# Performance work log

Measured on AMD Instinct MI355X. Metric: run time of the kernel, lower is better.

## Reference

```python
import jax, jax.numpy as jnp
import numpy as np

HID = 64
L = 3
RHO = 0.3
KMIN = 64
EPS = 1e-5


def conv1x1(x, w, b):
    # x: [B,C,H,W], w: [O,C], b: [O]
    return jnp.einsum('bchw,oc->bohw', x, w) + b[None, :, None, None]


def dwconv(x, w, pad, dil):
    # depthwise conv, w: [C,1,k,k], groups = C, no bias
    return jax.lax.conv_general_dilated(
        x, w, window_strides=(1, 1), padding=[(pad, pad), (pad, pad)],
        rhs_dilation=(dil, dil), feature_group_count=x.shape[1],
        dimension_numbers=('NCHW', 'OIHW', 'NCHW'))


def conv3x3(x, w, b):
    return jax.lax.conv_general_dilated(
        x, w, (1, 1), [(1, 1), (1, 1)],
        dimension_numbers=('NCHW', 'OIHW', 'NCHW')) + b[None, :, None, None]


def bn(x, g, b):
    # training-mode BatchNorm2d: batch statistics over (B,H,W) per channel
    mu = jnp.mean(x, axis=(0, 2, 3), keepdims=True)
    var = jnp.var(x, axis=(0, 2, 3), keepdims=True)
    return g[None, :, None, None] * (x - mu) * jax.lax.rsqrt(var + EPS) + b[None, :, None, None]


def setup_inputs() -> dict:
    key = jax.random.key(0)
    ks = jax.random.split(key, 40)
    B, C, H, W = 8, 1, 224, 224
    d = {}
    d['x'] = jax.random.normal(ks[0], (B, C, H, W), jnp.float32)
    # input_proj: 1x1 conv, out = 2*HID + L + 1 = 132
    d['w_in'] = jax.random.normal(ks[1], (2 * HID + L + 1, C), jnp.float32) * 0.5
    d['b_in'] = jnp.zeros((2 * HID + L + 1,), jnp.float32)
    for l in range(L):
        ksz = 2 * l + 3
        d[f'dw{l}'] = jax.random.normal(ks[2 + 4 * l], (HID, 1, ksz, ksz), jnp.float32) / ksz
        d[f'pw{l}_w'] = jax.random.normal(ks[3 + 4 * l], (HID, HID), jnp.float32) * (1.0 / np.sqrt(HID))
        d[f'pw{l}_b'] = jnp.zeros((HID,), jnp.float32)
        d[f'bn{l}_g'] = jnp.ones((HID,), jnp.float32)
        d[f'bn{l}_b'] = jnp.zeros((HID,), jnp.float32)
    d['imp_w1'] = jax.random.normal(ks[20], (HID // 4, HID), jnp.float32) * (1.0 / np.sqrt(HID))
    d['imp_b1'] = jnp.zeros((HID // 4,), jnp.float32)
    d['imp_w2'] = jax.random.normal(ks[21], (1, HID // 4, 3, 3), jnp.float32) * 0.1
    d['imp_b2'] = jnp.zeros((1,), jnp.float32)
    d['val_w'] = jax.random.normal(ks[22], (HID, HID), jnp.float32) * (1.0 / np.sqrt(HID))
    d['val_b'] = jnp.zeros((HID,), jnp.float32)
    d['out_w'] = jax.random.normal(ks[23], (HID, HID), jnp.float32) * (1.0 / np.sqrt(HID))
    d['out_b'] = jnp.zeros((HID,), jnp.float32)
    d['fin_w'] = jax.random.normal(ks[24], (HID, HID), jnp.float32) * (1.0 / np.sqrt(HID))
    d['fin_b'] = jnp.zeros((HID,), jnp.float32)
    return d


def reference(x, w_in, b_in,
              dw0, pw0_w, pw0_b, bn0_g, bn0_b,
              dw1, pw1_w, pw1_b, bn1_g, bn1_b,
              dw2, pw2_w, pw2_b, bn2_g, bn2_b,
              imp_w1, imp_b1, imp_w2, imp_b2,
              val_w, val_b, out_w, out_b, fin_w, fin_b):
    B, C, H, W = x.shape
    F_ = conv1x1(x, w_in, b_in)                       # [B, 2*HID+L+1, H, W]
    Q = F_[:, :HID]
    K = F_[:, HID:2 * HID]
    G = F_[:, 2 * HID:]                               # [B, L+1, H, W]
    # importance network: 1x1 conv -> ReLU -> 3x3 conv -> sigmoid
    imp = jax.nn.sigmoid(conv3x3(jax.nn.relu(conv1x1(K, imp_w1, imp_b1)), imp_w2, imp_b2))  # [B,1,H,W]
    # adaptive top-k sparsification: K = max(floor(rho*H*W), K_min)
    k = max(int(RHO * H * W), KMIN)
    mask_flat = imp.reshape(B, H * W)
    _, idx = jax.lax.top_k(mask_flat, k)              # [B, k]
    sparse = jnp.zeros_like(mask_flat).at[jnp.arange(B)[:, None], idx].set(1.0)
    K_cur = K * sparse.reshape(B, 1, H, W)
    # focal levels: kernel k_l = 2*l+3, dilation d_l = 2^l, pad = (k_l//2)*d_l
    levels = [(dw0, pw0_w, pw0_b, bn0_g, bn0_b, 1),
              (dw1, pw1_w, pw1_b, bn1_g, bn1_b, 2),
              (dw2, pw2_w, pw2_b, bn2_g, bn2_b, 4)]
    focal = []
    for dw, pw_w, pw_b, g, be, dil in levels:
        ksz = dw.shape[-1]
        pad = (ksz // 2) * dil
        K_cur = jax.nn.relu(bn(conv1x1(dwconv(K_cur, dw, pad, dil), pw_w, pw_b), g, be))
        focal.append(K_cur)
    Gn = jax.nn.softmax(G, axis=1)                    # softmax over L+1 gate channels
    K_agg = Gn[:, 0:1] * focal[0] + Gn[:, 1:2] * focal[1] + Gn[:, 2:3] * focal[2]
    K_global = jnp.mean(focal[-1], axis=(2, 3), keepdims=True)  # AdaptiveAvgPool2d(1), broadcast
    K_final = K_agg + Gn[:, -1:] * K_global
    V = conv1x1(K_final, val_w, val_b)
    QV = Q * V
    # output_proj Linear over channel dim (dropout is identity in eval)
    O = jnp.einsum('bchw,oc->bohw', QV, out_w) + out_b[None, :, None, None]
    # in_channels (1) != hidden_channels -> residual via final_conv on F[:, :HID] == Q
    x_proj = conv1x1(Q, fin_w, fin_b)
    return x_proj + O
```

## Files before the change

kernel.cpp:

```cpp
#include <hip/hip_runtime.h>

#define HDIM 224
#define WDIM 224
#define PPIX 50176
#define BATCH 8
#define NPIX 401408
#define KTOP 15052
#define NELEM 25690112
#define NBLK 6272
#define NBAND 14
#define NDWBLK 7168
#define NCHUNK 49

typedef __attribute__((ext_vector_type(8))) short bf8_t;
typedef __attribute__((ext_vector_type(4))) float f4_t;
typedef __attribute__((ext_vector_type(8))) unsigned short us8_t;
typedef __attribute__((ext_vector_type(4))) unsigned short us4_t;
#define MFMA_BF16 __builtin_amdgcn_mfma_f32_16x16x32_bf16

__device__ inline unsigned short f2bf(float f) {
    unsigned int u = __float_as_uint(f);
    return (unsigned short)((u + 0x7FFFu + ((u >> 16) & 1u)) >> 16);
}
__device__ inline float bf2f(unsigned short u) {
    return __uint_as_float(((unsigned int)u) << 16);
}

__device__ inline int ldsg(int r) { return ((r >> 3) ^ r) & 7; }

__device__ inline void stage_w64(const float* __restrict__ W, char* sWc, int t) {
    int o = t >> 2, cq = t & 3, c0 = cq * 16;
    const float4* src = (const float4*)(W + o * 64 + c0);
    float4 v0 = src[0], v1 = src[1], v2 = src[2], v3 = src[3];
    bf8_t p0, p1;
    p0[0] = (short)f2bf(v0.x); p0[1] = (short)f2bf(v0.y);
    p0[2] = (short)f2bf(v0.z); p0[3] = (short)f2bf(v0.w);
    p0[4] = (short)f2bf(v1.x); p0[5] = (short)f2bf(v1.y);
    p0[6] = (short)f2bf(v1.z); p0[7] = (short)f2bf(v1.w);
    p1[0] = (short)f2bf(v2.x); p1[1] = (short)f2bf(v2.y);
    p1[2] = (short)f2bf(v2.z); p1[3] = (short)f2bf(v2.w);
    p1[4] = (short)f2bf(v3.x); p1[5] = (short)f2bf(v3.y);
    p1[6] = (short)f2bf(v3.z); p1[7] = (short)f2bf(v3.w);
    int g = ldsg(o);
    *(bf8_t*)(sWc + o * 128 + (((2 * cq) ^ g) << 4)) = p0;
    *(bf8_t*)(sWc + o * 128 + (((2 * cq + 1) ^ g) << 4)) = p1;
}

__device__ inline void mfma64(const char* sWc, const char* sPc, int l, int m0, f4_t acc[4]) {
    int lr = l & 15, lg = l >> 4;
    int ra = m0 + lr, ga = ldsg(ra);
    const char* abase = sWc + ra * 128;
    bf8_t a0 = *(const bf8_t*)(abase + ((lg ^ ga) << 4));
    bf8_t a1 = *(const bf8_t*)(abase + (((lg + 4) ^ ga) << 4));
    #pragma unroll
    for (int nt = 0; nt < 4; nt++) {
        int rb = nt * 16 + lr, gb = ldsg(rb);
        const char* bbase = sPc + rb * 128;
        bf8_t b0 = *(const bf8_t*)(bbase + ((lg ^ gb) << 4));
        bf8_t b1 = *(const bf8_t*)(bbase + (((lg + 4) ^ gb) << 4));
        f4_t c = {0.f, 0.f, 0.f, 0.f};
        c = MFMA_BF16(a0, b0, c, 0, 0, 0);
        c = MFMA_BF16(a1, b1, c, 0, 0, 0);
        acc[nt] = c;
    }
}

__global__ __launch_bounds__(256) void prep_kernel(
    const float* __restrict__ w_in, const float* __restrict__ b_in,
    const float* __restrict__ imp_w1, const float* __restrict__ imp_b1,
    const float* __restrict__ fin_w, const float* __restrict__ fin_b,
    float* __restrict__ coeffs, unsigned int* __restrict__ ghist,
    unsigned int* __restrict__ pfx, int* __restrict__ rem)
{
    int t = threadIdx.x;
    if (t < 16) {
        float a = 0.f, d = 0.f;
        for (int c = 0; c < 64; c++) {
            a += imp_w1[t * 64 + c] * w_in[64 + c];
            d += imp_w1[t * 64 + c] * b_in[64 + c];
        }
        coeffs[t] = a;
        coeffs[16 + t] = d + imp_b1[t];
    }
    if (t < 64) {
        float a = 0.f, d = 0.f;
        for (int c = 0; c < 64; c++) {
            a += fin_w[t * 64 + c] * w_in[c];
            d += fin_w[t * 64 + c] * b_in[c];
        }
        coeffs[32 + t] = a;
        coeffs[96 + t] = d + fin_b[t];
    }
    for (int i = t; i < 2048; i += 256) ghist[i] = 0u;
    if (t < BATCH) { pfx[t] = 0u; rem[t] = KTOP; }
}

__global__ __launch_bounds__(256) void imp_kernel(
    const float* __restrict__ x, const float* __restrict__ coeffs,
    const float* __restrict__ imp_w2, const float* __restrict__ imp_b2,
    float* __restrict__ imp)
{
    int idx = blockIdx.x * 256 + threadIdx.x;
    int b = idx / PPIX, p = idx % PPIX;
    int h = p / WDIM, w = p % WDIM;
    float acc = imp_b2[0];
    #pragma unroll
    for (int ky = 0; ky < 3; ky++) {
        int hh = h + ky - 1;
        float okh = (hh >= 0 && hh < HDIM) ? 1.f : 0.f;
        int hc = min(max(hh, 0), HDIM - 1);
        #pragma unroll
        for (int kx = 0; kx < 3; kx++) {
            int ww = w + kx - 1;
            float ok = okh * ((ww >= 0 && ww < WDIM) ? 1.f : 0.f);
            int wc = min(max(ww, 0), WDIM - 1);
            float xv = x[b * PPIX + hc * WDIM + wc] * ok;
            #pragma unroll
            for (int c = 0; c < 16; c++) {
                float r = fmaxf(xv * coeffs[c] + coeffs[16 + c] * ok, 0.f);
                acc += r * imp_w2[c * 9 + ky * 3 + kx];
            }
        }
    }
    imp[idx] = 1.f / (1.f + expf(-acc));
}

__global__ __launch_bounds__(256) void topk_hist(
    const float* __restrict__ imp, const unsigned int* __restrict__ pfx,
    unsigned int* __restrict__ ghist, int shift)
{
    int b = blockIdx.x / NCHUNK, ch = blockIdx.x % NCHUNK;
    int t = threadIdx.x;
    __shared__ unsigned int hist[256];
    hist[t] = 0u;
    __syncthreads();
    unsigned int prefix = pfx[b];
    unsigned int himask = (shift == 24) ? 0u : (0xFFFFFFFFu << (shift + 8));
    float4 v = ((const float4*)(imp + b * PPIX + ch * 1024))[t];
    unsigned int bb[4] = {__float_as_uint(v.x), __float_as_uint(v.y),
                          __float_as_uint(v.z), __float_as_uint(v.w)};
    #pragma unroll
    for (int k = 0; k < 4; k++)
        if ((bb[k] & himask) == prefix)
            atomicAdd(&hist[(bb[k] >> shift) & 255u], 1u);
    __syncthreads();
    unsigned int c = hist[t];
    if (c) atomicAdd(&ghist[b * 256 + t], c);
}

__global__ __launch_bounds__(256) void topk_select(
    unsigned int* __restrict__ ghist, unsigned int* __restrict__ pfx,
    int* __restrict__ rem, int shift)
{
    int b = blockIdx.x;
    int t = threadIdx.x;
    __shared__ unsigned int h[256];
    h[t] = ghist[b * 256 + t];
    ghist[b * 256 + t] = 0u;
    __syncthreads();
    if (t == 0) {
        int r = rem[b];
        unsigned int bsel = 0u;
        for (int bin = 255; bin >= 0; bin--) {
            int c = (int)h[bin];
            if (c >= r) { bsel = (unsigned int)bin; break; }
            r -= c;
        }
        rem[b] = r;
        pfx[b] |= bsel << shift;
    }
}

__global__ __launch_bounds__(256) void topk_mask1(
    const float* __restrict__ imp, const unsigned int* __restrict__ pfx,
    float* __restrict__ mask, int* __restrict__ blocktie)
{
    int b = blockIdx.x / NCHUNK, ch = blockIdx.x % NCHUNK;
    int t = threadIdx.x;
    unsigned int T = pfx[b];
    float4 v = ((const float4*)(imp + b * PPIX + ch * 1024))[t];
    unsigned int bb[4] = {__float_as_uint(v.x), __float_as_uint(v.y),
                          __float_as_uint(v.z), __float_as_uint(v.w)};
    float4 mo;
    float* mp = &mo.x;
    int cnt = 0;
    #pragma unroll
    for (int k = 0; k < 4; k++) {
        mp[k] = (bb[k] > T) ? 1.f : 0.f;
        cnt += (bb[k] == T) ? 1 : 0;
    }
    ((float4*)(mask + b * PPIX + ch * 1024))[t] = mo;
    #pragma unroll
    for (int off = 32; off > 0; off >>= 1) cnt += __shfl_down(cnt, off);
    __shared__ int ws4[4];
    int lane = t & 63, wv = t >> 6;
    if (lane == 0) ws4[wv] = cnt;
    __syncthreads();
    if (t == 0) blocktie[b * NCHUNK + ch] = ws4[0] + ws4[1] + ws4[2] + ws4[3];
}

__global__ __launch_bounds__(256) void topk_mask2(
    const float* __restrict__ imp, const unsigned int* __restrict__ pfx,
    const int* __restrict__ rem_, const int* __restrict__ blocktie,
    float* __restrict__ mask)
{
    int b = blockIdx.x;
    int t = threadIdx.x, lane = t & 63, wv = t >> 6;
    unsigned int T = pfx[b];
    int rem = rem_[b];
    __shared__ int sbase[NCHUNK], scnt[NCHUNK];
    if (t == 0) {
        int s = 0;
        for (int i = 0; i < NCHUNK; i++) {
            sbase[i] = s;
            int c = blocktie[b * NCHUNK + i];
            scnt[i] = c;
            s += c;
        }
    }
    __syncthreads();
    __shared__ int wtot[4];
    for (int ch = 0; ch < NCHUNK; ch++) {
        if (scnt[ch] == 0) continue;
        int base = sbase[ch];
        if (base >= rem) break;
        for (int g = 0; g < 4; g++) {
            int i = b * PPIX + ch * 1024 + g * 256 + t;
            int flag = (__float_as_uint(imp[i]) == T) ? 1 : 0;
            unsigned long long bal = __ballot(flag);
            if (lane == 0) wtot[wv] = __popcll(bal);
            __syncthreads();
            int wbase = 0, tot = 0;
            for (int q = 0; q < 4; q++) { int c = wtot[q]; if (q < wv) wbase += c; tot += c; }
            if (flag && base + wbase + __popcll(bal & ((1ull << lane) - 1ull)) < rem)
                mask[i] = 1.f;
            base += tot;
            __syncthreads();
        }
    }
}

__global__ __launch_bounds__(256, 4) void level0_kernel(
    const float* __restrict__ x, const float* __restrict__ mask,
    const float* __restrict__ w_in, const float* __restrict__ b_in,
    const float* __restrict__ dw_w, const float* __restrict__ pw_w,
    const float* __restrict__ pw_b,
    unsigned short* __restrict__ y_out, float* __restrict__ partials)
{
    __shared__ __align__(16) short sW[4096];
    __shared__ __align__(16) short sP[4096];
    __shared__ float sred[128];
    __shared__ float sBias[64];
    char* sWc = (char*)sW; char* sPc = (char*)sP;
    int t = threadIdx.x;
    int swz = (blockIdx.x & 7) * 784 + (blockIdx.x >> 3);
    int b = swz / 784;
    int l = t & 63, og = t >> 6;
    int p0 = (swz % 784) * 64;
    int p = p0 + l;
    int h = p / WDIM, w = p % WDIM;
    stage_w64(pw_w, sWc, t);
    if (t < 64) sBias[t] = pw_b[t];

    int rowoff[3]; float okhf[3];
    int wcs[3]; float okwf[3];
    #pragma unroll
    for (int k = 0; k < 3; k++) {
        int hh = h + k - 1;
        okhf[k] = (hh >= 0 && hh < HDIM) ? 1.f : 0.f;
        rowoff[k] = min(max(hh, 0), HDIM - 1) * WDIM;
        int ww = w + k - 1;
        okwf[k] = (ww >= 0 && ww < WDIM) ? 1.f : 0.f;
        wcs[k] = min(max(ww, 0), WDIM - 1);
    }
    float mv[9], mxv[9];
    const float* mb = mask + b * PPIX;
    const float* xb = x + b * PPIX;
    #pragma unroll
    for (int ky = 0; ky < 3; ky++) {
        #pragma unroll
        for (int kx = 0; kx < 3; kx++) {
            int a = rowoff[ky] + wcs[kx];
            float mm = mb[a] * (okhf[ky] * okwf[kx]);
            mv[ky * 3 + kx] = mm;
            mxv[ky * 3 + kx] = mm * xb[a];
        }
    }
    bf8_t pk0, pk1;
    #pragma unroll
    for (int j = 0; j < 16; j++) {
        int c = og * 16 + j;
        float wk = w_in[64 + c], bk = b_in[64 + c];
        const float* dwr = dw_w + c * 9;
        float a0 = 0.f, a1 = 0.f;
        #pragma unroll
        for (int tp = 0; tp < 9; tp++) {
            float dv = dwr[tp];
            a0 += dv * mxv[tp];
            a1 += dv * mv[tp];
        }
        unsigned short bv = f2bf(wk * a0 + bk * a1);
        if (j < 8) pk0[j] = (short)bv; else pk1[j - 8] = (short)bv;
    }
    int gl = ldsg(l);
    *(bf8_t*)(sPc + l * 128 + (((2 * og) ^ gl) << 4)) = pk0;
    *(bf8_t*)(sPc + l * 128 + (((2 * og + 1) ^ gl) << 4)) = pk1;
    __syncthreads();

    int m0 = og * 16, lr = l & 15, lg = l >> 4;
    f4_t acc[4];
    mfma64(sWc, sPc, l, m0, acc);
    unsigned short* ybase = y_out + (size_t)b * 64 * PPIX + p0;
    #pragma unroll
    for (int r = 0; r < 4; r++) {
        int o = m0 + 4 * lg + r;
        float bias = sBias[o];
        float s = 0.f, s2 = 0.f;
        #pragma unroll
        for (int nt = 0; nt < 4; nt++) {
            float yv = acc[nt][r] + bias;
            ybase[(size_t)o * PPIX + nt * 16 + lr] = f2bf(yv);
            s += yv; s2 += yv * yv;
        }
        #pragma unroll
        for (int m = 1; m < 16; m <<= 1) {
            s += __shfl_xor(s, m);
            s2 += __shfl_xor(s2, m);
        }
        if (lr == 0) { sred[2 * o] = s; sred[2 * o + 1] = s2; }
    }
    __syncthreads();
    if (t < 128) partials[(size_t)blockIdx.x * 128 + t] = sred[t];
}

template<int KSZ, int DIL>
__global__ __launch_bounds__(256, 3) void dw_kernel(
    const unsigned short* __restrict__ in, const float* __restrict__ bnp,
    const float* __restrict__ dw_w, unsigned short* __restrict__ out)
{
    constexpr int PAD = (KSZ / 2) * DIL;
    constexpr int BH = 16;
    constexpr int LR = BH + 2 * PAD;
    constexpr int SW = WDIM + 2 * PAD + 4;
    constexpr int SEG = 16 + 2 * PAD;
    __shared__ float sIn[LR * SW];

    int t = threadIdx.x;
    int swz = (blockIdx.x & 7) * (NDWBLK / 8) + (blockIdx.x >> 3);
    int bc = swz / NBAND, band = swz % NBAND;
    int c = bc & 63;
    int r0 = band * BH;
    float sc = bnp[c], sh = bnp[64 + c];
    const unsigned short* plane = in + (size_t)bc * PPIX;

    constexpr int PADC = SW - WDIM;
    for (int i = t; i < LR * PADC; i += 256) {
        int r = i / PADC, cc = i % PADC;
        int col = (cc < PAD) ? cc : (cc + WDIM);
        sIn[r * SW + col] = 0.f;
    }
    for (int i = t; i < LR * 28; i += 256) {
        int sr = i / 28, q = i % 28;
        int gr = r0 - PAD + sr;
        float4 a = {0.f, 0.f, 0.f, 0.f}, bq = {0.f, 0.f, 0.f, 0.f};
        if (gr >= 0 && gr < HDIM) {
            us8_t v = *(const us8_t*)(plane + gr * WDIM + 8 * q);
            a.x = fmaxf(sc * bf2f(v[0]) + sh, 0.f);
            a.y = fmaxf(sc * bf2f(v[1]) + sh, 0.f);
            a.z = fmaxf(sc * bf2f(v[2]) + sh, 0.f);
            a.w = fmaxf(sc * bf2f(v[3]) + sh, 0.f);
            bq.x = fmaxf(sc * bf2f(v[4]) + sh, 0.f);
            bq.y = fmaxf(sc * bf2f(v[5]) + sh, 0.f);
            bq.z = fmaxf(sc * bf2f(v[6]) + sh, 0.f);
            bq.w = fmaxf(sc * bf2f(v[7]) + sh, 0.f);
        }
        *(float4*)(sIn + sr * SW + PAD + 8 * q) = a;
        *(float4*)(sIn + sr * SW + PAD + 8 * q + 4) = bq;
    }
    __syncthreads();

    if (t < 224) {
        const float* dwr = dw_w + c * KSZ * KSZ;
        float wk[KSZ * KSZ];
        #pragma unroll
        for (int i = 0; i < KSZ * KSZ; i++) wk[i] = dwr[i];

        int xs = t % 14, row = t / 14;
        int x0 = xs * 16;
        float acc[16];
        #pragma unroll
        for (int j = 0; j < 16; j++) acc[j] = 0.f;
        #pragma unroll
        for (int ky = 0; ky < KSZ; ky++) {
            const float4* srow = (const float4*)(sIn + (row + ky * DIL) * SW + x0);
            float s[SEG];
            #pragma unroll
            for (int i = 0; i < SEG / 4; i++) ((float4*)s)[i] = srow[i];
            #pragma unroll
            for (int kx = 0; kx < KSZ; kx++) {
                float wv = wk[ky * KSZ + kx];
                #pragma unroll
                for (int j = 0; j < 16; j++)
                    acc[j] += s[j + DIL * kx] * wv;
            }
        }
        us8_t o0, o1;
        #pragma unroll
        for (int j = 0; j < 8; j++) { o0[j] = f2bf(acc[j]); o1[j] = f2bf(acc[8 + j]); }
        unsigned short* orow = out + (size_t)bc * PPIX + (r0 + row) * WDIM + x0;
        *(us8_t*)orow = o0;
        *(us8_t*)(orow + 8) = o1;
    }
}

__global__ __launch_bounds__(256, 4) void pw_kernel(
    const float* __restrict__ pw_w, const float* __restrict__ pw_b,
    const unsigned short* __restrict__ src_y, unsigned short* __restrict__ dst_y,
    float* __restrict__ partials)
{
    __shared__ __align__(16) short sW[4096];
    __shared__ __align__(16) short sP[4096];
    __shared__ float sred[128];
    __shared__ float sBias[64];
    char* sWc = (char*)sW; char* sPc = (char*)sP;
    int t = threadIdx.x;
    int swz = (blockIdx.x & 7) * 784 + (blockIdx.x >> 3);
    int b = swz / 784;
    int p0 = (swz % 784) * 64;
    stage_w64(pw_w, sWc, t);
    if (t < 64) sBias[t] = pw_b[t];

    const unsigned short* sbase_g = src_y + (size_t)b * 64 * PPIX + p0;
    unsigned short* dbase_g = dst_y + (size_t)b * 64 * PPIX + p0;
    {
        int c = t >> 2, pg = t & 3;
        const unsigned short* src = sbase_g + (size_t)c * PPIX + 16 * pg;
        us8_t v0 = *(const us8_t*)src;
        us8_t v1 = *(const us8_t*)(src + 8);
        int kc = c >> 3, cb = 2 * (c & 7);
        #pragma unroll
        for (int e = 0; e < 16; e++) {
            int r = 16 * pg + e;
            int gr = ldsg(r);
            unsigned short val = (e < 8) ? (unsigned short)v0[e] : (unsigned short)v1[e - 8];
            *(unsigned short*)(sPc + r * 128 + ((kc ^ gr) << 4) + cb) = val;
        }
    }
    __syncthreads();

    int l = t & 63, wv = t >> 6, m0 = wv * 16;
    int lr = l & 15, lg = l >> 4;
    f4_t acc[4];
    mfma64(sWc, sPc, l, m0, acc);
    #pragma unroll
    for (int r = 0; r < 4; r++) {
        int o = m0 + 4 * lg + r;
        float bias = sBias[o];
        float s = 0.f, s2 = 0.f;
        #pragma unroll
        for (int nt = 0; nt < 4; nt++) {
            float yv = acc[nt][r] + bias;
            dbase_g[(size_t)o * PPIX + nt * 16 + lr] = f2bf(yv);
            s += yv; s2 += yv * yv;
        }
        #pragma unroll
        for (int m = 1; m < 16; m <<= 1) {
            s += __shfl_xor(s, m);
            s2 += __shfl_xor(s2, m);
        }
        if (lr == 0) { sred[2 * o] = s; sred[2 * o + 1] = s2; }
    }
    __syncthreads();
    if (t < 128) partials[(size_t)blockIdx.x * 128 + t] = sred[t];
}

__global__ __launch_bounds__(256) void bnfin_kernel(
    const float* __restrict__ partials,
    const float* __restrict__ g, const float* __restrict__ be,
    float* __restrict__ bnp)
{
    int c = blockIdx.x;
    int t = threadIdx.x;
    float s = 0.f, s2 = 0.f;
    for (int blk = t; blk < NBLK; blk += 256) {
        s  += partials[(size_t)blk * 128 + 2 * c];
        s2 += partials[(size_t)blk * 128 + 2 * c + 1];
    }
    #pragma unroll
    for (int off = 32; off > 0; off >>= 1) {
        s += __shfl_down(s, off);
        s2 += __shfl_down(s2, off);
    }
    __shared__ float wsm[8];
    int lane = t & 63, wv = t >> 6;
    if (lane == 0) { wsm[wv] = s; wsm[4 + wv] = s2; }
    __syncthreads();
    if (t == 0) {
        s = wsm[0] + wsm[1] + wsm[2] + wsm[3];
        s2 = wsm[4] + wsm[5] + wsm[6] + wsm[7];
        const float inv_n = 1.f / (float)NPIX;
        float mu = s * inv_n;
        float var = s2 * inv_n - mu * mu;
        float sc = g[c] * rsqrtf(var + 1e-5f);
        bnp[c] = sc;
        bnp[64 + c] = be[c] - mu * sc;
    }
}

__global__ __launch_bounds__(1024) void kglobal_kernel(
    const unsigned short* __restrict__ y2, const float* __restrict__ bnp2,
    float* __restrict__ kg)
{
    int bc = blockIdx.x;
    int c = bc & 63;
    int t = threadIdx.x;
    const unsigned short* row = y2 + (size_t)bc * PPIX;
    float sc = bnp2[c], sh = bnp2[64 + c];
    float s = 0.f;
    for (int ii = t; ii < PPIX / 8; ii += 1024) {
        us8_t v = *(const us8_t*)(row + 8 * ii);
        #pragma unroll
        for (int k = 0; k < 8; k++) s += fmaxf(sc * bf2f(v[k]) + sh, 0.f);
    }
    #pragma unroll
    for (int off = 32; off > 0; off >>= 1) s += __shfl_down(s, off);
    __shared__ float wsum[16];
    int lane = t & 63, wv = t >> 6;
    if (lane == 0) wsum[wv] = s;
    __syncthreads();
    if (t == 0) {
        float tot = 0.f;
        #pragma unroll
        for (int q = 0; q < 16; q++) tot += wsum[q];
        kg[bc] = tot * (1.f / (float)PPIX);
    }
}

__global__ __launch_bounds__(256, 4) void final_kernel(
    const float* __restrict__ x, const float* __restrict__ w_in,
    const float* __restrict__ b_in,
    const unsigned short* __restrict__ y0, const unsigned short* __restrict__ y1,
    const unsigned short* __restrict__ y2,
    const float* __restrict__ bnp, const float* __restrict__ kg,
    const float* __restrict__ val_w, const float* __restrict__ val_b,
    const float* __restrict__ out_w, const float* __restrict__ out_b,
    const float* __restrict__ coeffs, float* __restrict__ out)
{
    __shared__ __align__(16) short sVW[4096];
    __shared__ __align__(16) short sOW[4096];
    __shared__ __align__(16) short sP[4096];
    __shared__ float sxv[64], sQW[64], sQB[64], sVB[64], sOB[64], sC1[64], sC2[64];
    char* sVWc = (char*)sVW; char* sOWc = (char*)sOW; char* sPc = (char*)sP;
    int t = threadIdx.x;
    int blk = blockIdx.x;
    int b = blk / 784;
    int l = t & 63, wv = t >> 6;
    int p0 = (blk % 784) * 64;
    stage_w64(val_w, sVWc, t);
    stage_w64(out_w, sOWc, t);
    if (t < 64) {
        sQW[t] = w_in[t]; sQB[t] = b_in[t];
        sVB[t] = val_b[t]; sOB[t] = out_b[t];
        sC1[t] = coeffs[32 + t]; sC2[t] = coeffs[96 + t];
    }

    float xv = x[b * PPIX + p0 + l];
    if (wv == 0) sxv[l] = xv;
    float g0 = xv * w_in[128] + b_in[128];
    float g1 = xv * w_in[129] + b_in[129];
    float g2 = xv * w_in[130] + b_in[130];
    float g3 = xv * w_in[131] + b_in[131];
    float mx = fmaxf(fmaxf(g0, g1), fmaxf(g2, g3));
    float e0 = expf(g0 - mx), e1 = expf(g1 - mx), e2 = expf(g2 - mx), e3 = expf(g3 - mx);
    float inv = 1.f / (e0 + e1 + e2 + e3);
    float G0 = e0 * inv, G1 = e1 * inv, G2 = e2 * inv, G3 = e3 * inv;

    bf8_t pk0, pk1;
    #pragma unroll
    for (int j = 0; j < 16; j++) {
        int c = wv * 16 + j;
        size_t idx = (size_t)(b * 64 + c) * PPIX + p0 + l;
        float f0 = fmaxf(bnp[c] * bf2f(y0[idx]) + bnp[64 + c], 0.f);
        float f1 = fmaxf(bnp[128 + c] * bf2f(y1[idx]) + bnp[192 + c], 0.f);
        float f2 = fmaxf(bnp[256 + c] * bf2f(y2[idx]) + bnp[320 + c], 0.f);
        float kf = G0 * f0 + G1 * f1 + G2 * f2 + G3 * kg[b * 64 + c];
        unsigned short bv = f2bf(kf);
        if (j < 8) pk0[j] = (short)bv; else pk1[j - 8] = (short)bv;
    }
    int gl = ldsg(l);
    *(bf8_t*)(sPc + l * 128 + (((2 * wv) ^ gl) << 4)) = pk0;
    *(bf8_t*)(sPc + l * 128 + (((2 * wv + 1) ^ gl) << 4)) = pk1;
    __syncthreads();

    int m0 = wv * 16, lr = l & 15, lg = l >> 4;
    f4_t accV[4];
    mfma64(sVWc, sPc, l, m0, accV);
    __syncthreads();

    #pragma unroll
    for (int nt = 0; nt < 4; nt++) {
        float xvp = sxv[nt * 16 + lr];
        us4_t q4;
        #pragma unroll
        for (int r = 0; r < 4; r++) {
            int o = m0 + 4 * lg + r;
            float V = accV[nt][r] + sVB[o];
            float q = xvp * sQW[o] + sQB[o];
            q4[r] = f2bf(q * V);
        }
        int rb = nt * 16 + lr, gb = ldsg(rb);
        int kc = 2 * wv + (lg >> 1);
        *(us4_t*)(sPc + rb * 128 + ((kc ^ gb) << 4) + 8 * (lg & 1)) = q4;
    }
    __syncthreads();

    f4_t accO[4];
    mfma64(sOWc, sPc, l, m0, accO);
    #pragma unroll
    for (int nt = 0; nt < 4; nt++) {
        float xvp = sxv[nt * 16 + lr];
        #pragma unroll
        for (int r = 0; r < 4; r++) {
            int o = m0 + 4 * lg + r;
            out[(size_t)(b * 64 + o) * PPIX + p0 + nt * 16 + lr] =
                accO[nt][r] + sOB[o] + xvp * sC1[o] + sC2[o];
        }
    }
}

extern "C" void kernel_launch(void* const* d_in, const int* in_sizes, int n_in,
                              void* d_out, int out_size, void* d_ws, size_t ws_size,
                              hipStream_t stream)
{
    (void)in_sizes; (void)n_in; (void)out_size; (void)ws_size;
    const float* x      = (const float*)d_in[0];
    const float* w_in   = (const float*)d_in[1];
    const float* b_in   = (const float*)d_in[2];
    const float* dw0    = (const float*)d_in[3];
    const float* pw0_w  = (const float*)d_in[4];
    const float* pw0_b  = (const float*)d_in[5];
    const float* bn0_g  = (const float*)d_in[6];
    const float* bn0_b  = (const float*)d_in[7];
    const float* dw1    = (const float*)d_in[8];
    const float* pw1_w  = (const float*)d_in[9];
    const float* pw1_b  = (const float*)d_in[10];
    const float* bn1_g  = (const float*)d_in[11];
    const float* bn1_b  = (const float*)d_in[12];
    const float* dw2    = (const float*)d_in[13];
    const float* pw2_w  = (const float*)d_in[14];
    const float* pw2_b  = (const float*)d_in[15];
    const float* bn2_g  = (const float*)d_in[16];
    const float* bn2_b  = (const float*)d_in[17];
    const float* imp_w1 = (const float*)d_in[18];
    const float* imp_b1 = (const float*)d_in[19];
    const float* imp_w2 = (const float*)d_in[20];
    const float* imp_b2 = (const float*)d_in[21];
    const float* val_w  = (const float*)d_in[22];
    const float* val_b  = (const float*)d_in[23];
    const float* out_w  = (const float*)d_in[24];
    const float* out_b  = (const float*)d_in[25];
    const float* fin_w  = (const float*)d_in[26];
    const float* fin_b  = (const float*)d_in[27];

    unsigned short* y0 = (unsigned short*)d_ws;
    unsigned short* y1 = y0 + (size_t)NELEM;
    unsigned short* y2 = y1 + (size_t)NELEM;
    unsigned short* yt = y2 + (size_t)NELEM;
    float* imp  = (float*)(yt + (size_t)NELEM);
    float* mask = imp + NPIX;
    float* partials = mask + NPIX;
    float* bnp   = partials + (size_t)NBLK * 128;
    float* kg    = bnp + 384;
    float* coeffs = kg + 512;
    unsigned int* ghist = (unsigned int*)(coeffs + 160);
    unsigned int* pfx   = ghist + 2048;
    int* rem            = (int*)(pfx + 8);
    int* blocktie       = rem + 8;
    float* outp = (float*)d_out;

    prep_kernel<<<1, 256, 0, stream>>>(w_in, b_in, imp_w1, imp_b1, fin_w, fin_b,
                                       coeffs, ghist, pfx, rem);
    imp_kernel<<<NPIX / 256, 256, 0, stream>>>(x, coeffs, imp_w2, imp_b2, imp);

    for (int shift = 24; shift >= 0; shift -= 8) {
        topk_hist<<<BATCH * NCHUNK, 256, 0, stream>>>(imp, pfx, ghist, shift);
        topk_select<<<BATCH, 256, 0, stream>>>(ghist, pfx, rem, shift);
    }
    topk_mask1<<<BATCH * NCHUNK, 256, 0, stream>>>(imp, pfx, mask, blocktie);
    topk_mask2<<<BATCH, 256, 0, stream>>>(imp, pfx, rem, blocktie, mask);

    level0_kernel<<<NBLK, 256, 0, stream>>>(x, mask, w_in, b_in, dw0, pw0_w, pw0_b,
                                            y0, partials);
    bnfin_kernel<<<64, 256, 0, stream>>>(partials, bn0_g, bn0_b, bnp);

    dw_kernel<5, 2><<<NDWBLK, 256, 0, stream>>>(y0, bnp, dw1, yt);
    pw_kernel<<<NBLK, 256, 0, stream>>>(pw1_w, pw1_b, yt, y1, partials);
    bnfin_kernel<<<64, 256, 0, stream>>>(partials, bn1_g, bn1_b, bnp + 128);

    dw_kernel<7, 4><<<NDWBLK, 256, 0, stream>>>(y1, bnp + 128, dw2, yt);
    pw_kernel<<<NBLK, 256, 0, stream>>>(pw2_w, pw2_b, yt, y2, partials);
    bnfin_kernel<<<64, 256, 0, stream>>>(partials, bn2_g, bn2_b, bnp + 256);

    kglobal_kernel<<<512, 1024, 0, stream>>>(y2, bnp + 256, kg);
    final_kernel<<<NBLK, 256, 0, stream>>>(x, w_in, b_in, y0, y1, y2, bnp, kg,
                                           val_w, val_b, out_w, out_b, coeffs, outp);
}
```

Before: 388.9 us.

## Fuse radix top-k into one per-batch kernel and vectorize final loads

Replaces the ten-launch radix-select top-k (histogram/select per byte plus two mask passes) with a single kernel using one 1024-thread block per batch image. Each block runs all four radix passes and the tie-breaking mask pass with per-wave LDS histograms. The final kernel also now loads y0/y1/y2 as 16-element vectors per channel and precomputes gate softmax in shared memory. Launch overhead and global atomics go away, but only 8 blocks run the top-k, so its serial bandwidth is limited.

New measurement: 428.9 us. 10.3% more time.

```diff
diff --git a/kernel.cpp b/kernel.cpp
--- a/kernel.cpp
+++ b/kernel.cpp
@@ -10,7 +10,6 @@
 #define NBLK 6272
 #define NBAND 14
 #define NDWBLK 7168
-#define NCHUNK 49
 
 typedef __attribute__((ext_vector_type(8))) short bf8_t;
 typedef __attribute__((ext_vector_type(4))) float f4_t;
@@ -69,8 +68,7 @@
     const float* __restrict__ w_in, const float* __restrict__ b_in,
     const float* __restrict__ imp_w1, const float* __restrict__ imp_b1,
     const float* __restrict__ fin_w, const float* __restrict__ fin_b,
-    float* __restrict__ coeffs, unsigned int* __restrict__ ghist,
-    unsigned int* __restrict__ pfx, int* __restrict__ rem)
+    float* __restrict__ coeffs)
 {
     int t = threadIdx.x;
     if (t < 16) {
@@ -91,8 +89,6 @@
         coeffs[32 + t] = a;
         coeffs[96 + t] = d + fin_b[t];
     }
-    for (int i = t; i < 2048; i += 256) ghist[i] = 0u;
-    if (t < BATCH) { pfx[t] = 0u; rem[t] = KTOP; }
 }
 
 __global__ __launch_bounds__(256) void imp_kernel(
@@ -125,118 +121,75 @@
     imp[idx] = 1.f / (1.f + expf(-acc));
 }
 
-__global__ __launch_bounds__(256) void topk_hist(
-    const float* __restrict__ imp, const unsigned int* __restrict__ pfx,
-    unsigned int* __restrict__ ghist, int shift)
-{
-    int b = blockIdx.x / NCHUNK, ch = blockIdx.x % NCHUNK;
-    int t = threadIdx.x;
+__global__ __launch_bounds__(1024) void topk_kernel(
+    const float* __restrict__ imp, float* __restrict__ mask)
+{
+    int b = blockIdx.x;
+    const float* v = imp + b * PPIX;
+    float* m = mask + b * PPIX;
+    int t = threadIdx.x;
+    int lane = t & 63, wv = t >> 6;
+    __shared__ unsigned int whist[16][256];
     __shared__ unsigned int hist[256];
-    hist[t] = 0u;
-    __syncthreads();
-    unsigned int prefix = pfx[b];
-    unsigned int himask = (shift == 24) ? 0u : (0xFFFFFFFFu << (shift + 8));
-    float4 v = ((const float4*)(imp + b * PPIX + ch * 1024))[t];
-    unsigned int bb[4] = {__float_as_uint(v.x), __float_as_uint(v.y),
-                          __float_as_uint(v.z), __float_as_uint(v.w)};
-    #pragma unroll
-    for (int k = 0; k < 4; k++)
-        if ((bb[k] & himask) == prefix)
-            atomicAdd(&hist[(bb[k] >> shift) & 255u], 1u);
-    __syncthreads();
-    unsigned int c = hist[t];
-    if (c) atomicAdd(&ghist[b * 256 + t], c);
-}
-
-__global__ __launch_bounds__(256) void topk_select(
-    unsigned int* __restrict__ ghist, unsigned int* __restrict__ pfx,
-    int* __restrict__ rem, int shift)
-{
-    int b = blockIdx.x;
-    int t = threadIdx.x;
-    __shared__ unsigned int h[256];
-    h[t] = ghist[b * 256 + t];
-    ghist[b * 256 + t] = 0u;
-    __syncthreads();
-    if (t == 0) {
-        int r = rem[b];
-        unsigned int bsel = 0u;
-        for (int bin = 255; bin >= 0; bin--) {
-            int c = (int)h[bin];
-            if (c >= r) { bsel = (unsigned int)bin; break; }
-            r -= c;
-        }
-        rem[b] = r;
-        pfx[b] |= bsel << shift;
-    }
-}
-
-__global__ __launch_bounds__(256) void topk_mask1(
-    const float* __restrict__ imp, const unsigned int* __restrict__ pfx,
-    float* __restrict__ mask, int* __restrict__ blocktie)
-{
-    int b = blockIdx.x / NCHUNK, ch = blockIdx.x % NCHUNK;
-    int t = threadIdx.x;
-    unsigned int T = pfx[b];
-    float4 v = ((const float4*)(imp + b * PPIX + ch * 1024))[t];
-    unsigned int bb[4] = {__float_as_uint(v.x), __float_as_uint(v.y),
-                          __float_as_uint(v.z), __float_as_uint(v.w)};
-    float4 mo;
-    float* mp = &mo.x;
-    int cnt = 0;
-    #pragma unroll
-    for (int k = 0; k < 4; k++) {
-        mp[k] = (bb[k] > T) ? 1.f : 0.f;
-        cnt += (bb[k] == T) ? 1 : 0;
-    }
-    ((float4*)(mask + b * PPIX + ch * 1024))[t] = mo;
-    #pragma unroll
-    for (int off = 32; off > 0; off >>= 1) cnt += __shfl_down(cnt, off);
-    __shared__ int ws4[4];
-    int lane = t & 63, wv = t >> 6;
-    if (lane == 0) ws4[wv] = cnt;
-    __syncthreads();
-    if (t == 0) blocktie[b * NCHUNK + ch] = ws4[0] + ws4[1] + ws4[2] + ws4[3];
-}
-
-__global__ __launch_bounds__(256) void topk_mask2(
-    const float* __restrict__ imp, const unsigned int* __restrict__ pfx,
-    const int* __restrict__ rem_, const int* __restrict__ blocktie,
-    float* __restrict__ mask)
-{
-    int b = blockIdx.x;
-    int t = threadIdx.x, lane = t & 63, wv = t >> 6;
-    unsigned int T = pfx[b];
-    int rem = rem_[b];
-    __shared__ int sbase[NCHUNK], scnt[NCHUNK];
-    if (t == 0) {
-        int s = 0;
-        for (int i = 0; i < NCHUNK; i++) {
-            sbase[i] = s;
-            int c = blocktie[b * NCHUNK + i];
-            scnt[i] = c;
-            s += c;
-        }
-    }
-    __syncthreads();
-    __shared__ int wtot[4];
-    for (int ch = 0; ch < NCHUNK; ch++) {
-        if (scnt[ch] == 0) continue;
-        int base = sbase[ch];
-        if (base >= rem) break;
-        for (int g = 0; g < 4; g++) {
-            int i = b * PPIX + ch * 1024 + g * 256 + t;
-            int flag = (__float_as_uint(imp[i]) == T) ? 1 : 0;
-            unsigned long long bal = __ballot(flag);
-            if (lane == 0) wtot[wv] = __popcll(bal);
-            __syncthreads();
-            int wbase = 0, tot = 0;
-            for (int q = 0; q < 4; q++) { int c = wtot[q]; if (q < wv) wbase += c; tot += c; }
-            if (flag && base + wbase + __popcll(bal & ((1ull << lane) - 1ull)) < rem)
-                mask[i] = 1.f;
-            base += tot;
-            __syncthreads();
-        }
+    __shared__ unsigned int sh_prefix;
+    __shared__ int sh_rem;
+    __shared__ int wtot[16];
+
+    unsigned int prefix = 0u;
+    int remaining = KTOP;
+    for (int pass = 0; pass < 4; pass++) {
+        int shift = 24 - 8 * pass;
+        for (int i = t; i < 4096; i += 1024) ((unsigned int*)whist)[i] = 0u;
+        __syncthreads();
+        unsigned int himask = (pass == 0) ? 0u : (0xFFFFFFFFu << (shift + 8));
+        for (int i = t; i < PPIX; i += 1024) {
+            unsigned int bits = __float_as_uint(v[i]);
+            if ((bits & himask) == prefix)
+                atomicAdd(&whist[wv][(bits >> shift) & 255u], 1u);
+        }
+        __syncthreads();
+        if (t < 256) {
+            unsigned int s = 0u;
+            #pragma unroll
+            for (int q = 0; q < 16; q++) s += whist[q][t];
+            hist[t] = s;
+        }
+        __syncthreads();
+        if (t == 0) {
+            int r = remaining;
+            unsigned int bsel = 0u;
+            for (int bin = 255; bin >= 0; bin--) {
+                int c = (int)hist[bin];
+                if (c >= r) { bsel = (unsigned int)bin; break; }
+                r -= c;
+            }
+            sh_rem = r;
+            sh_prefix = prefix | (bsel << shift);
+        }
+        __syncthreads();
+        prefix = sh_prefix;
+        remaining = sh_rem;
+    }
+
+    unsigned int T = prefix;
+    int base = 0;
+    for (int i0 = 0; i0 < PPIX; i0 += 1024) {
+        int i = i0 + t;
+        unsigned int bits = __float_as_uint(v[i]);
+        int flag = (bits == T) ? 1 : 0;
+        unsigned long long bal = __ballot(flag);
+        if (lane == 0) wtot[wv] = __popcll(bal);
+        __syncthreads();
+        int wbase = 0, tot = 0;
+        #pragma unroll
+        for (int q = 0; q < 16; q++) { int c = wtot[q]; if (q < wv) wbase += c; tot += c; }
+        int excl = wbase + __popcll(bal & ((1ull << lane) - 1ull));
+        float mout = 0.f;
+        if (bits > T) mout = 1.f;
+        else if (flag && (base + excl) < remaining) mout = 1.f;
+        m[i] = mout;
+        base += tot;
+        __syncthreads();
     }
 }
 
@@ -549,7 +502,8 @@
     __shared__ __align__(16) short sVW[4096];
     __shared__ __align__(16) short sOW[4096];
     __shared__ __align__(16) short sP[4096];
-    __shared__ float sxv[64], sQW[64], sQB[64], sVB[64], sOB[64], sC1[64], sC2[64];
+    __shared__ float sxv[64], sG[320];
+    __shared__ float sQW[64], sQB[64], sVB[64], sOB[64], sC1[64], sC2[64];
     char* sVWc = (char*)sVW; char* sOWc = (char*)sOW; char* sPc = (char*)sP;
     int t = threadIdx.x;
     int blk = blockIdx.x;
@@ -562,34 +516,52 @@
         sQW[t] = w_in[t]; sQB[t] = b_in[t];
         sVB[t] = val_b[t]; sOB[t] = out_b[t];
         sC1[t] = coeffs[32 + t]; sC2[t] = coeffs[96 + t];
-    }
-
-    float xv = x[b * PPIX + p0 + l];
-    if (wv == 0) sxv[l] = xv;
-    float g0 = xv * w_in[128] + b_in[128];
-    float g1 = xv * w_in[129] + b_in[129];
-    float g2 = xv * w_in[130] + b_in[130];
-    float g3 = xv * w_in[131] + b_in[131];
-    float mx = fmaxf(fmaxf(g0, g1), fmaxf(g2, g3));
-    float e0 = expf(g0 - mx), e1 = expf(g1 - mx), e2 = expf(g2 - mx), e3 = expf(g3 - mx);
-    float inv = 1.f / (e0 + e1 + e2 + e3);
-    float G0 = e0 * inv, G1 = e1 * inv, G2 = e2 * inv, G3 = e3 * inv;
-
-    bf8_t pk0, pk1;
-    #pragma unroll
-    for (int j = 0; j < 16; j++) {
-        int c = wv * 16 + j;
-        size_t idx = (size_t)(b * 64 + c) * PPIX + p0 + l;
-        float f0 = fmaxf(bnp[c] * bf2f(y0[idx]) + bnp[64 + c], 0.f);
-        float f1 = fmaxf(bnp[128 + c] * bf2f(y1[idx]) + bnp[192 + c], 0.f);
-        float f2 = fmaxf(bnp[256 + c] * bf2f(y2[idx]) + bnp[320 + c], 0.f);
-        float kf = G0 * f0 + G1 * f1 + G2 * f2 + G3 * kg[b * 64 + c];
-        unsigned short bv = f2bf(kf);
-        if (j < 8) pk0[j] = (short)bv; else pk1[j - 8] = (short)bv;
-    }
-    int gl = ldsg(l);
-    *(bf8_t*)(sPc + l * 128 + (((2 * wv) ^ gl) << 4)) = pk0;
-    *(bf8_t*)(sPc + l * 128 + (((2 * wv + 1) ^ gl) << 4)) = pk1;
+        float xv = x[b * PPIX + p0 + t];
+        sxv[t] = xv;
+        float g0 = xv * w_in[128] + b_in[128];
+        float g1 = xv * w_in[129] + b_in[129];
+        float g2 = xv * w_in[130] + b_in[130];
+        float g3 = xv * w_in[131] + b_in[131];
+        float mx = fmaxf(fmaxf(g0, g1), fmaxf(g2, g3));
+        float e0 = expf(g0 - mx), e1 = expf(g1 - mx);
+        float e2 = expf(g2 - mx), e3 = expf(g3 - mx);
+        float inv = 1.f / (e0 + e1 + e2 + e3);
+        sG[5 * t + 0] = e0 * inv;
+        sG[5 * t + 1] = e1 * inv;
+        sG[5 * t + 2] = e2 * inv;
+        sG[5 * t + 3] = e3 * inv;
+    }
+    __syncthreads();
+
+    {
+        int c = t >> 2, pg = t & 3;
+        size_t base = (size_t)(b * 64 + c) * PPIX + p0 + 16 * pg;
+        us8_t a0 = *(const us8_t*)(y0 + base);
+        us8_t a1 = *(const us8_t*)(y0 + base + 8);
+        us8_t q0 = *(const us8_t*)(y1 + base);
+        us8_t q1 = *(const us8_t*)(y1 + base + 8);
+        us8_t r0 = *(const us8_t*)(y2 + base);
+        us8_t r1 = *(const us8_t*)(y2 + base + 8);
+        float s0 = bnp[c],       h0 = bnp[64 + c];
+        float s1 = bnp[128 + c], h1 = bnp[192 + c];
+        float s2 = bnp[256 + c], h2 = bnp[320 + c];
+        float kgc = kg[b * 64 + c];
+        int kc = c >> 3, cb = 2 * (c & 7);
+        #pragma unroll
+        for (int e = 0; e < 16; e++) {
+            unsigned short u0 = (e < 8) ? (unsigned short)a0[e] : (unsigned short)a1[e - 8];
+            unsigned short u1 = (e < 8) ? (unsigned short)q0[e] : (unsigned short)q1[e - 8];
+            unsigned short u2 = (e < 8) ? (unsigned short)r0[e] : (unsigned short)r1[e - 8];
+            float f0 = fmaxf(s0 * bf2f(u0) + h0, 0.f);
+            float f1 = fmaxf(s1 * bf2f(u1) + h1, 0.f);
+            float f2 = fmaxf(s2 * bf2f(u2) + h2, 0.f);
+            int r = 16 * pg + e;
+            float kf = sG[5 * r] * f0 + sG[5 * r + 1] * f1
+                     + sG[5 * r + 2] * f2 + sG[5 * r + 3] * kgc;
+            int gr = ldsg(r);
+            *(unsigned short*)(sPc + r * 128 + ((kc ^ gr) << 4) + cb) = f2bf(kf);
+        }
+    }
     __syncthreads();
 
     int m0 = wv * 16, lr = l & 15, lg = l >> 4;
@@ -672,22 +644,12 @@
     float* bnp   = partials + (size_t)NBLK * 128;
     float* kg    = bnp + 384;
     float* coeffs = kg + 512;
-    unsigned int* ghist = (unsigned int*)(coeffs + 160);
-    unsigned int* pfx   = ghist + 2048;
-    int* rem            = (int*)(pfx + 8);
-    int* blocktie       = rem + 8;
     float* outp = (float*)d_out;
 
     prep_kernel<<<1, 256, 0, stream>>>(w_in, b_in, imp_w1, imp_b1, fin_w, fin_b,
-                                       coeffs, ghist, pfx, rem);
+                                       coeffs);
     imp_kernel<<<NPIX / 256, 256, 0, stream>>>(x, coeffs, imp_w2, imp_b2, imp);
-
-    for (int shift = 24; shift >= 0; shift -= 8) {
-        topk_hist<<<BATCH * NCHUNK, 256, 0, stream>>>(imp, pfx, ghist, shift);
-        topk_select<<<BATCH, 256, 0, stream>>>(ghist, pfx, rem, shift);
-    }
-    topk_mask1<<<BATCH * NCHUNK, 256, 0, stream>>>(imp, pfx, mask, blocktie);
-    topk_mask2<<<BATCH, 256, 0, stream>>>(imp, pfx, rem, blocktie, mask);
+    topk_kernel<<<BATCH, 1024, 0, stream>>>(imp, mask);
 
     level0_kernel<<<NBLK, 256, 0, stream>>>(x, mask, w_in, b_in, dw0, pw0_w, pw0_b,
                                             y0, partials);
```
